# Optimization experiments

Hardware: AMD Instinct MI355X
Metric: run time of the kernel (lower is better)

The kernel has to match this reference:

```python
import jax, jax.numpy as jnp
import numpy as np

NT, NTR, NQ = 2048, 4096, 257  # time samples, traces, quantile knots


def cumtrapz(y, dx):
    # cumulative trapezoid along last axis, zero-prepended (preserve_dims=True)
    c = jnp.cumsum((y[..., 1:] + y[..., :-1]) * (0.5 * dx), axis=-1)
    return jnp.concatenate([jnp.zeros_like(y[..., :1]), c], axis=-1)


def trapz(y, dx):
    return (jnp.sum(y, axis=-1) - 0.5 * (y[..., 0] + y[..., -1])) * dx


def renorm(f, dx):
    # square + normalize to a pdf along time (standard W2-FWI renormalization)
    g = f * f
    return g / trapz(g, dx)[..., None]


def true_quantile(pdf, x, p, dx):
    # step-function quantile: invert clipped CDF via searchsorted per trace
    cdf = jnp.clip(cumtrapz(pdf, dx), 0.0, 1.0)  # [B, nt]
    idx = jax.vmap(lambda c: jnp.searchsorted(c, p))(cdf)  # [B, nq]
    idx = jnp.clip(idx, 0, x.shape[0] - 1)
    return x[idx]  # [B, nq]


def natural_cubic_coeffs(p, q):
    # batched natural cubic spline of q(p); knots p shared across batch
    h = p[1:] - p[:-1]                                 # [n-1]
    slope = (q[..., 1:] - q[..., :-1]) / h             # [B, n-1]
    rhs = 6.0 * (slope[..., 1:] - slope[..., :-1])     # [B, n-2]
    diag = 2.0 * (h[:-1] + h[1:])
    off = h[1:-1]
    T = jnp.diag(diag) + jnp.diag(off, 1) + jnp.diag(off, -1)  # [n-2, n-2], shared
    M_inner = jnp.linalg.solve(T, rhs[..., None])[..., 0]      # [B, n-2]
    z = jnp.zeros_like(q[..., :1])
    M = jnp.concatenate([z, M_inner, z], axis=-1)      # natural BCs: M0 = Mn = 0
    a = q[..., :-1]
    b = slope - h * (2.0 * M[..., :-1] + M[..., 1:]) / 6.0
    c = 0.5 * M[..., :-1]
    d = (M[..., 1:] - M[..., :-1]) / (6.0 * h)
    return a, b, c, d  # each [B, n-1]


def spline_eval(p, a, b, c, d, tq):
    # vectorized batched spline evaluation (replaces per-element Python loop)
    idx = jnp.clip(jnp.searchsorted(p, tq, side='left') - 1, 0, p.shape[0] - 2)
    frac = tq - p[idx]
    ga = jnp.take_along_axis(a, idx, axis=-1)
    gb = jnp.take_along_axis(b, idx, axis=-1)
    gc = jnp.take_along_axis(c, idx, axis=-1)
    gd = jnp.take_along_axis(d, idx, axis=-1)
    return ga + frac * (gb + frac * (gc + frac * gd))


def w2_forward(f, obs_data, t, p):
    dx = t[1] - t[0]
    # constructor-time part: quantile splines of observed data
    q = true_quantile(renorm(obs_data, dx), t, p, dx)   # [B, nq]
    a, b, c, d = natural_cubic_coeffs(p, q)
    # forward: CDF of synthetic, composed with observed quantile
    F = cumtrapz(renorm(f, dx), dx)                     # [B, nt]
    off_diag = spline_eval(p, a, b, c, d, F)            # [B, nt]
    diff = (t[None, :] - off_diag) ** 2
    integrated = trapz(diff * f, dx)                    # [B]
    return jnp.sum(integrated)


def setup_inputs() -> dict:
    key = jax.random.key(0)
    k1, k2 = jax.random.split(key)
    f = jax.random.normal(k1, (NTR, NT), dtype=jnp.float32)
    obs_data = jax.random.normal(k2, (NTR, NT), dtype=jnp.float32)
    t = jnp.linspace(0.0, 2.0, NT, dtype=jnp.float32)
    p = jnp.linspace(0.0, 1.0, NQ, dtype=jnp.float32)
    return {"f": f, "obs_data": obs_data, "t": t, "p": p}


def reference(f, obs_data, t, p):
    return w2_forward(f, obs_data, t, p)
```

## Files before the change

kernel.cpp:

```cpp
#include <hip/hip_runtime.h>

#define TPB 256
#define NT_ 2048
#define NQ_ 257
#define EPT 8
#define BW 16
#define BD (2*BW+1)
#define BAND_BYTES (BD*256*4)
#define H_P 0.00390625

__device__ __forceinline__ double shfl_down_f64(double x, int off) {
  union { double d; int i[2]; } u; u.d = x;
  u.i[0] = __shfl_down(u.i[0], off, 64);
  u.i[1] = __shfl_down(u.i[1], off, 64);
  return u.d;
}

__global__ void w2_setup(float* __restrict__ bandS) {
  __shared__ double sh_L[256];
  __shared__ double sh_winv[256];
  const int tid = threadIdx.x;
  if (tid < 255) {
    double d, dm;
    if (tid >= 20) {
      d = dm = 3.7320508075688772935;
    } else {
      d = 4.0; dm = 0.0;
      for (int i = 1; i <= tid; i++) { dm = d; d = 4.0 - 1.0 / d; }
    }
    sh_winv[tid] = 256.0 / d;
    sh_L[tid] = (tid == 0) ? 0.0 : 1.0 / dm;
  }
  __syncthreads();
  const int j = tid;
  const double H = H_P;
  if (j < 255) {
    double y[BW + 1];
    y[0] = 1.0;
    #pragma unroll
    for (int m = 1; m <= BW; m++) {
      int i = j + m;
      y[m] = (i <= 254) ? (-sh_L[i] * y[m - 1]) : 0.0;
    }
    double xn = 0.0;
    #pragma unroll
    for (int m = BW; m >= 0; m--) {
      int i = j + m;
      double val = 0.0;
      if (i <= 254) {
        double num = y[m] - ((i < 254) ? H * xn : 0.0);
        val = num * sh_winv[i];
        xn = val;
      }
      bandS[(m + BW) * 256 + j] = (float)val;
    }
    #pragma unroll
    for (int m = -1; m >= -BW; m--) {
      int i = j + m;
      double val = 0.0;
      if (i >= 0) {
        val = (-H * xn) * sh_winv[i];
        xn = val;
      }
      bandS[(m + BW) * 256 + j] = (float)val;
    }
  } else {
    for (int mm = 0; mm < BD; mm++) bandS[mm * 256 + j] = 0.0f;
  }
}

__global__ __launch_bounds__(TPB) void w2_main(
    const float* __restrict__ f, const float* __restrict__ obs,
    const float* __restrict__ t, const float* __restrict__ bandS,
    double* __restrict__ row_out) {
  __shared__ float s_q[NQ_];
  __shared__ float s_rhs[255 + 2 * BW];
  __shared__ float s_M[NQ_];
  __shared__ float4 s_coef[256];
  __shared__ float s_wf[4];
  __shared__ float s_wf2[4];
  __shared__ double s_wd[4];
  __shared__ double s_misc[2];

  const int tid = threadIdx.x;
  const int lane = tid & 63;
  const int wid = tid >> 6;
  const int row = blockIdx.x;
  const int base = tid * EPT;
  const int emax = (tid == TPB - 1) ? EPT - 1 : EPT;

  const double dx = (double)t[1] - (double)t[0];

  float tl[EPT + 1];
  {
    const float4 a = *reinterpret_cast<const float4*>(t + base);
    const float4 b = *reinterpret_cast<const float4*>(t + base + 4);
    tl[0] = a.x; tl[1] = a.y; tl[2] = a.z; tl[3] = a.w;
    tl[4] = b.x; tl[5] = b.y; tl[6] = b.z; tl[7] = b.w;
  }
  tl[EPT] = (tid < TPB - 1) ? t[base + EPT] : 0.0f;

  float sA[EPT];
  float ep = 0.0f;
  {
    const float* orow = obs + (size_t)row * NT_;
    float ov[EPT + 1];
    const float4 a = *reinterpret_cast<const float4*>(orow + base);
    const float4 b = *reinterpret_cast<const float4*>(orow + base + 4);
    ov[0] = a.x; ov[1] = a.y; ov[2] = a.z; ov[3] = a.w;
    ov[4] = b.x; ov[5] = b.y; ov[6] = b.z; ov[7] = b.w;
    ov[EPT] = (tid < TPB - 1) ? orow[base + EPT] : 0.0f;
    for (int k = 0; k < emax; k++) {
      sA[k] = ov[k] * ov[k] + ov[k + 1] * ov[k + 1];
      ep += sA[k];
    }
    if (emax < EPT) sA[EPT - 1] = 0.0f;
  }
  float v = ep;
  #pragma unroll
  for (int off = 1; off < 64; off <<= 1) {
    float w = __shfl_up(v, off, 64);
    if (lane >= off) v += w;
  }
  float excl = __shfl_up(v, 1, 64);
  if (lane == 0) excl = 0.0f;
  if (lane == 63) s_wf[wid] = v;
  __syncthreads();
  float woff = 0.0f, tot = 0.0f;
  #pragma unroll
  for (int w = 0; w < 4; w++) {
    float sw = s_wf[w];
    if (w < wid) woff += sw;
    tot += sw;
  }
  float run = woff + excl;
  float incl = woff + v;
  float inv = 1.0f / tot;

  {
    float cprev = fminf(run * inv, 1.0f);
    int j = (int)(cprev * 256.0f) + 1;
    float r = run;
    for (int k = 0; k < emax; k++) {
      float cu_uns = (k == emax - 1) ? incl : (r + sA[k]);
      r = cu_uns;
      float cuc = fminf(cu_uns * inv, 1.0f);
      int jh = (int)(cuc * 256.0f);
      float tq = tl[k + 1];
      for (; j <= jh; j++) s_q[j] = tq;
    }
    if (tid == 0) s_q[0] = tl[0];
    if (tid == TPB - 1) {
      float tq = tl[EPT - 1];
      for (; j <= 256; j++) s_q[j] = tq;
    }
  }

  const float* frow = f + (size_t)row * NT_;
  float fv[EPT + 1];
  {
    const float4 a = *reinterpret_cast<const float4*>(frow + base);
    const float4 b = *reinterpret_cast<const float4*>(frow + base + 4);
    fv[0] = a.x; fv[1] = a.y; fv[2] = a.z; fv[3] = a.w;
    fv[4] = b.x; fv[5] = b.y; fv[6] = b.z; fv[7] = b.w;
  }
  fv[EPT] = (tid < TPB - 1) ? frow[base + EPT] : 0.0f;

  float sB[EPT];
  float ep2 = 0.0f;
  for (int k = 0; k < emax; k++) {
    sB[k] = fv[k] * fv[k] + fv[k + 1] * fv[k + 1];
    ep2 += sB[k];
  }
  if (emax < EPT) sB[EPT - 1] = 0.0f;
  float v2 = ep2;
  #pragma unroll
  for (int off = 1; off < 64; off <<= 1) {
    float w = __shfl_up(v2, off, 64);
    if (lane >= off) v2 += w;
  }
  float excl2 = __shfl_up(v2, 1, 64);
  if (lane == 0) excl2 = 0.0f;
  if (lane == 63) s_wf2[wid] = v2;
  __syncthreads();

  float woff2 = 0.0f, tot2 = 0.0f;
  #pragma unroll
  for (int w = 0; w < 4; w++) {
    float sw = s_wf2[w];
    if (w < wid) woff2 += sw;
    tot2 += sw;
  }
  float run2 = woff2 + excl2;
  float inv2 = 1.0f / tot2;

  if (tid < 255) {
    float sl0 = (s_q[tid + 1] - s_q[tid]) * 256.0f;
    float sl1 = (s_q[tid + 2] - s_q[tid + 1]) * 256.0f;
    s_rhs[BW + tid] = 6.0f * (sl1 - sl0);
  }
  if (tid < BW) s_rhs[tid] = 0.0f;
  if (tid >= TPB - BW) s_rhs[tid + (2 * BW - 1)] = 0.0f;
  __syncthreads();

  float Mreg = 0.0f;
  if (tid < 255) {
    #pragma unroll 11
    for (int dd = 0; dd < BD; dd++)
      Mreg += bandS[dd * 256 + tid] * s_rhs[tid + dd];
  }
  if (tid < 255) s_M[tid + 1] = Mreg;
  if (tid == 0) { s_M[0] = 0.0f; s_M[256] = 0.0f; }
  __syncthreads();

  {
    const float h = (float)H_P;
    float q0 = s_q[tid], q1 = s_q[tid + 1];
    float Mi = s_M[tid], Mi1 = s_M[tid + 1];
    float sl = (q1 - q0) * 256.0f;
    float b = sl - h * (2.0f * Mi + Mi1) * (1.0f / 6.0f);
    float c = 0.5f * Mi;
    float d = (Mi1 - Mi) * (256.0f / 6.0f);
    s_coef[tid] = make_float4(q0, b, c, d);
  }
  __syncthreads();

  double wsum = 0.0;
  {
    float r2 = run2;
    #pragma unroll
    for (int k = 0; k < EPT; k++) {
      if (k > 0) r2 += sB[k - 1];
      float F = r2 * inv2;
      float G = F * 256.0f;
      int idx = (int)ceilf(G) - 1;
      if (idx < 0) idx = 0;
      if (idx > 255) idx = 255;
      float frac = F - (float)idx * (float)H_P;
      float4 cf = s_coef[idx];
      float val = cf.x + frac * (cf.y + frac * (cf.z + frac * cf.w));
      float diff = tl[k] - val;
      float wv = diff * diff * fv[k];
      if (tid == 0 && k == 0) s_misc[0] = (double)wv;
      if (tid == TPB - 1 && k == EPT - 1) s_misc[1] = (double)wv;
      wsum += (double)wv;
    }
  }
  double rv = wsum;
  #pragma unroll
  for (int off = 32; off >= 1; off >>= 1) rv += shfl_down_f64(rv, off);
  if (lane == 0) s_wd[wid] = rv;
  __syncthreads();
  if (tid == 0) {
    double totw = s_wd[0] + s_wd[1] + s_wd[2] + s_wd[3];
    row_out[row] = (totw - 0.5 * (s_misc[0] + s_misc[1])) * dx;
  }
}

__global__ void w2_reduce(const double* __restrict__ row_out, int ntr,
                          float* __restrict__ out) {
  __shared__ double s[TPB];
  int tid = threadIdx.x;
  double v = 0.0;
  for (int i = tid; i < ntr; i += TPB) v += row_out[i];
  s[tid] = v; __syncthreads();
  for (int off = TPB / 2; off > 0; off >>= 1) {
    if (tid < off) s[tid] += s[tid + off];
    __syncthreads();
  }
  if (tid == 0) out[0] = (float)s[0];
}

extern "C" void kernel_launch(void* const* d_in, const int* in_sizes, int n_in,
                              void* d_out, int out_size, void* d_ws, size_t ws_size,
                              hipStream_t stream) {
  const float* f   = (const float*)d_in[0];
  const float* obs = (const float*)d_in[1];
  const float* t   = (const float*)d_in[2];
  int nt = in_sizes[2];
  int ntr = in_sizes[0] / nt;

  float* bandS = (float*)d_ws;
  double* rows = (double*)((char*)d_ws + BAND_BYTES);

  hipLaunchKernelGGL(w2_setup, dim3(1), dim3(256), 0, stream, bandS);
  hipLaunchKernelGGL(w2_main, dim3(ntr), dim3(TPB), 0, stream,
                     f, obs, t, bandS, rows);
  hipLaunchKernelGGL(w2_reduce, dim3(1), dim3(TPB), 0, stream,
                     rows, ntr, (float*)d_out);
}
```

Measured before the change: 43.92 us.

## Process two traces per block and use shuffle-based final reduction

```diff
diff --git a/kernel.cpp b/kernel.cpp
--- a/kernel.cpp
+++ b/kernel.cpp
@@ -8,6 +8,7 @@
 #define BD (2*BW+1)
 #define BAND_BYTES (BD*256*4)
 #define H_P 0.00390625
+#define RTPB 1024
 
 __device__ __forceinline__ double shfl_down_f64(double x, int off) {
   union { double d; int i[2]; } u; u.d = x;
@@ -73,19 +74,19 @@
     const float* __restrict__ f, const float* __restrict__ obs,
     const float* __restrict__ t, const float* __restrict__ bandS,
     double* __restrict__ row_out) {
-  __shared__ float s_q[NQ_];
-  __shared__ float s_rhs[255 + 2 * BW];
-  __shared__ float s_M[NQ_];
-  __shared__ float4 s_coef[256];
-  __shared__ float s_wf[4];
-  __shared__ float s_wf2[4];
-  __shared__ double s_wd[4];
-  __shared__ double s_misc[2];
+  __shared__ float s_qA[NQ_], s_qB[NQ_];
+  __shared__ float s_rhsA[255 + 2 * BW], s_rhsB[255 + 2 * BW];
+  __shared__ float s_MA[NQ_], s_MB[NQ_];
+  __shared__ float4 s_coefA[256], s_coefB[256];
+  __shared__ float s_wfA[4], s_wfB[4], s_wf2A[4], s_wf2B[4];
+  __shared__ double s_wdA[4], s_wdB[4];
+  __shared__ double s_miscA[2], s_miscB[2];
 
   const int tid = threadIdx.x;
   const int lane = tid & 63;
   const int wid = tid >> 6;
-  const int row = blockIdx.x;
+  const int rowA = (int)blockIdx.x * 2;
+  const int rowB = rowA + 1;
   const int base = tid * EPT;
   const int emax = (tid == TPB - 1) ? EPT - 1 : EPT;
 
@@ -100,175 +101,242 @@
   }
   tl[EPT] = (tid < TPB - 1) ? t[base + EPT] : 0.0f;
 
-  float sA[EPT];
-  float ep = 0.0f;
-  {
-    const float* orow = obs + (size_t)row * NT_;
-    float ov[EPT + 1];
-    const float4 a = *reinterpret_cast<const float4*>(orow + base);
-    const float4 b = *reinterpret_cast<const float4*>(orow + base + 4);
-    ov[0] = a.x; ov[1] = a.y; ov[2] = a.z; ov[3] = a.w;
-    ov[4] = b.x; ov[5] = b.y; ov[6] = b.z; ov[7] = b.w;
-    ov[EPT] = (tid < TPB - 1) ? orow[base + EPT] : 0.0f;
+  float sAA[EPT], sAB[EPT];
+  float epA = 0.0f, epB = 0.0f;
+  {
+    const float* orA = obs + (size_t)rowA * NT_;
+    const float* orB = obs + (size_t)rowB * NT_;
+    float ovA[EPT + 1], ovB[EPT + 1];
+    {
+      const float4 a0 = *reinterpret_cast<const float4*>(orA + base);
+      const float4 a1 = *reinterpret_cast<const float4*>(orA + base + 4);
+      const float4 b0 = *reinterpret_cast<const float4*>(orB + base);
+      const float4 b1 = *reinterpret_cast<const float4*>(orB + base + 4);
+      ovA[0] = a0.x; ovA[1] = a0.y; ovA[2] = a0.z; ovA[3] = a0.w;
+      ovA[4] = a1.x; ovA[5] = a1.y; ovA[6] = a1.z; ovA[7] = a1.w;
+      ovB[0] = b0.x; ovB[1] = b0.y; ovB[2] = b0.z; ovB[3] = b0.w;
+      ovB[4] = b1.x; ovB[5] = b1.y; ovB[6] = b1.z; ovB[7] = b1.w;
+    }
+    ovA[EPT] = (tid < TPB - 1) ? orA[base + EPT] : 0.0f;
+    ovB[EPT] = (tid < TPB - 1) ? orB[base + EPT] : 0.0f;
     for (int k = 0; k < emax; k++) {
-      sA[k] = ov[k] * ov[k] + ov[k + 1] * ov[k + 1];
-      ep += sA[k];
-    }
-    if (emax < EPT) sA[EPT - 1] = 0.0f;
-  }
-  float v = ep;
+      sAA[k] = ovA[k] * ovA[k] + ovA[k + 1] * ovA[k + 1];
+      sAB[k] = ovB[k] * ovB[k] + ovB[k + 1] * ovB[k + 1];
+      epA += sAA[k];
+      epB += sAB[k];
+    }
+    if (emax < EPT) { sAA[EPT - 1] = 0.0f; sAB[EPT - 1] = 0.0f; }
+  }
+  float vA = epA, vB = epB;
   #pragma unroll
   for (int off = 1; off < 64; off <<= 1) {
-    float w = __shfl_up(v, off, 64);
-    if (lane >= off) v += w;
-  }
-  float excl = __shfl_up(v, 1, 64);
-  if (lane == 0) excl = 0.0f;
-  if (lane == 63) s_wf[wid] = v;
-  __syncthreads();
-  float woff = 0.0f, tot = 0.0f;
+    float wA = __shfl_up(vA, off, 64);
+    float wB = __shfl_up(vB, off, 64);
+    if (lane >= off) { vA += wA; vB += wB; }
+  }
+  float exclA = __shfl_up(vA, 1, 64);
+  float exclB = __shfl_up(vB, 1, 64);
+  if (lane == 0) { exclA = 0.0f; exclB = 0.0f; }
+  if (lane == 63) { s_wfA[wid] = vA; s_wfB[wid] = vB; }
+  __syncthreads();
+  float woffA = 0.0f, totA = 0.0f, woffB = 0.0f, totB = 0.0f;
   #pragma unroll
   for (int w = 0; w < 4; w++) {
-    float sw = s_wf[w];
-    if (w < wid) woff += sw;
-    tot += sw;
-  }
-  float run = woff + excl;
-  float incl = woff + v;
-  float inv = 1.0f / tot;
-
-  {
-    float cprev = fminf(run * inv, 1.0f);
+    float swA = s_wfA[w], swB = s_wfB[w];
+    if (w < wid) { woffA += swA; woffB += swB; }
+    totA += swA; totB += swB;
+  }
+  float runA = woffA + exclA, inclA = woffA + vA, invA = 1.0f / totA;
+  float runB = woffB + exclB, inclB = woffB + vB, invB = 1.0f / totB;
+
+  {
+    float cprev = fminf(runA * invA, 1.0f);
     int j = (int)(cprev * 256.0f) + 1;
-    float r = run;
+    float r = runA;
     for (int k = 0; k < emax; k++) {
-      float cu_uns = (k == emax - 1) ? incl : (r + sA[k]);
+      float cu_uns = (k == emax - 1) ? inclA : (r + sAA[k]);
       r = cu_uns;
-      float cuc = fminf(cu_uns * inv, 1.0f);
+      float cuc = fminf(cu_uns * invA, 1.0f);
       int jh = (int)(cuc * 256.0f);
       float tq = tl[k + 1];
-      for (; j <= jh; j++) s_q[j] = tq;
-    }
-    if (tid == 0) s_q[0] = tl[0];
+      for (; j <= jh; j++) s_qA[j] = tq;
+    }
+    if (tid == 0) s_qA[0] = tl[0];
     if (tid == TPB - 1) {
       float tq = tl[EPT - 1];
-      for (; j <= 256; j++) s_q[j] = tq;
-    }
-  }
-
-  const float* frow = f + (size_t)row * NT_;
-  float fv[EPT + 1];
-  {
-    const float4 a = *reinterpret_cast<const float4*>(frow + base);
-    const float4 b = *reinterpret_cast<const float4*>(frow + base + 4);
-    fv[0] = a.x; fv[1] = a.y; fv[2] = a.z; fv[3] = a.w;
-    fv[4] = b.x; fv[5] = b.y; fv[6] = b.z; fv[7] = b.w;
-  }
-  fv[EPT] = (tid < TPB - 1) ? frow[base + EPT] : 0.0f;
-
-  float sB[EPT];
-  float ep2 = 0.0f;
+      for (; j <= 256; j++) s_qA[j] = tq;
+    }
+  }
+  {
+    float cprev = fminf(runB * invB, 1.0f);
+    int j = (int)(cprev * 256.0f) + 1;
+    float r = runB;
+    for (int k = 0; k < emax; k++) {
+      float cu_uns = (k == emax - 1) ? inclB : (r + sAB[k]);
+      r = cu_uns;
+      float cuc = fminf(cu_uns * invB, 1.0f);
+      int jh = (int)(cuc * 256.0f);
+      float tq = tl[k + 1];
+      for (; j <= jh; j++) s_qB[j] = tq;
+    }
+    if (tid == 0) s_qB[0] = tl[0];
+    if (tid == TPB - 1) {
+      float tq = tl[EPT - 1];
+      for (; j <= 256; j++) s_qB[j] = tq;
+    }
+  }
+
+  const float* frA = f + (size_t)rowA * NT_;
+  const float* frB = f + (size_t)rowB * NT_;
+  float fvA[EPT + 1], fvB[EPT + 1];
+  {
+    const float4 a0 = *reinterpret_cast<const float4*>(frA + base);
+    const float4 a1 = *reinterpret_cast<const float4*>(frA + base + 4);
+    const float4 b0 = *reinterpret_cast<const float4*>(frB + base);
+    const float4 b1 = *reinterpret_cast<const float4*>(frB + base + 4);
+    fvA[0] = a0.x; fvA[1] = a0.y; fvA[2] = a0.z; fvA[3] = a0.w;
+    fvA[4] = a1.x; fvA[5] = a1.y; fvA[6] = a1.z; fvA[7] = a1.w;
+    fvB[0] = b0.x; fvB[1] = b0.y; fvB[2] = b0.z; fvB[3] = b0.w;
+    fvB[4] = b1.x; fvB[5] = b1.y; fvB[6] = b1.z; fvB[7] = b1.w;
+  }
+  fvA[EPT] = (tid < TPB - 1) ? frA[base + EPT] : 0.0f;
+  fvB[EPT] = (tid < TPB - 1) ? frB[base + EPT] : 0.0f;
+
+  float sBA[EPT], sBB[EPT];
+  float ep2A = 0.0f, ep2B = 0.0f;
   for (int k = 0; k < emax; k++) {
-    sB[k] = fv[k] * fv[k] + fv[k + 1] * fv[k + 1];
-    ep2 += sB[k];
-  }
-  if (emax < EPT) sB[EPT - 1] = 0.0f;
-  float v2 = ep2;
+    sBA[k] = fvA[k] * fvA[k] + fvA[k + 1] * fvA[k + 1];
+    sBB[k] = fvB[k] * fvB[k] + fvB[k + 1] * fvB[k + 1];
+    ep2A += sBA[k];
+    ep2B += sBB[k];
+  }
+  if (emax < EPT) { sBA[EPT - 1] = 0.0f; sBB[EPT - 1] = 0.0f; }
+  float v2A = ep2A, v2B = ep2B;
   #pragma unroll
   for (int off = 1; off < 64; off <<= 1) {
-    float w = __shfl_up(v2, off, 64);
-    if (lane >= off) v2 += w;
-  }
-  float excl2 = __shfl_up(v2, 1, 64);
-  if (lane == 0) excl2 = 0.0f;
-  if (lane == 63) s_wf2[wid] = v2;
-  __syncthreads();
-
-  float woff2 = 0.0f, tot2 = 0.0f;
+    float wA = __shfl_up(v2A, off, 64);
+    float wB = __shfl_up(v2B, off, 64);
+    if (lane >= off) { v2A += wA; v2B += wB; }
+  }
+  float excl2A = __shfl_up(v2A, 1, 64);
+  float excl2B = __shfl_up(v2B, 1, 64);
+  if (lane == 0) { excl2A = 0.0f; excl2B = 0.0f; }
+  if (lane == 63) { s_wf2A[wid] = v2A; s_wf2B[wid] = v2B; }
+  __syncthreads();
+
+  float woff2A = 0.0f, tot2A = 0.0f, woff2B = 0.0f, tot2B = 0.0f;
   #pragma unroll
   for (int w = 0; w < 4; w++) {
-    float sw = s_wf2[w];
-    if (w < wid) woff2 += sw;
-    tot2 += sw;
-  }
-  float run2 = woff2 + excl2;
-  float inv2 = 1.0f / tot2;
+    float swA = s_wf2A[w], swB = s_wf2B[w];
+    if (w < wid) { woff2A += swA; woff2B += swB; }
+    tot2A += swA; tot2B += swB;
+  }
+  float run2A = woff2A + excl2A, inv2A = 1.0f / tot2A;
+  float run2B = woff2B + excl2B, inv2B = 1.0f / tot2B;
 
   if (tid < 255) {
-    float sl0 = (s_q[tid + 1] - s_q[tid]) * 256.0f;
-    float sl1 = (s_q[tid + 2] - s_q[tid + 1]) * 256.0f;
-    s_rhs[BW + tid] = 6.0f * (sl1 - sl0);
-  }
-  if (tid < BW) s_rhs[tid] = 0.0f;
-  if (tid >= TPB - BW) s_rhs[tid + (2 * BW - 1)] = 0.0f;
-  __syncthreads();
-
-  float Mreg = 0.0f;
+    float sl0A = (s_qA[tid + 1] - s_qA[tid]) * 256.0f;
+    float sl1A = (s_qA[tid + 2] - s_qA[tid + 1]) * 256.0f;
+    s_rhsA[BW + tid] = 6.0f * (sl1A - sl0A);
+    float sl0B = (s_qB[tid + 1] - s_qB[tid]) * 256.0f;
+    float sl1B = (s_qB[tid + 2] - s_qB[tid + 1]) * 256.0f;
+    s_rhsB[BW + tid] = 6.0f * (sl1B - sl0B);
+  }
+  if (tid < BW) { s_rhsA[tid] = 0.0f; s_rhsB[tid] = 0.0f; }
+  if (tid >= TPB - BW) {
+    s_rhsA[tid + (2 * BW - 1)] = 0.0f;
+    s_rhsB[tid + (2 * BW - 1)] = 0.0f;
+  }
+  __syncthreads();
+
+  float MregA = 0.0f, MregB = 0.0f;
   if (tid < 255) {
     #pragma unroll 11
-    for (int dd = 0; dd < BD; dd++)
-      Mreg += bandS[dd * 256 + tid] * s_rhs[tid + dd];
-  }
-  if (tid < 255) s_M[tid + 1] = Mreg;
-  if (tid == 0) { s_M[0] = 0.0f; s_M[256] = 0.0f; }
+    for (int dd = 0; dd < BD; dd++) {
+      float w = bandS[dd * 256 + tid];
+      MregA += w * s_rhsA[tid + dd];
+      MregB += w * s_rhsB[tid + dd];
+    }
+  }
+  if (tid < 255) { s_MA[tid + 1] = MregA; s_MB[tid + 1] = MregB; }
+  if (tid == 0) { s_MA[0] = 0.0f; s_MA[256] = 0.0f; s_MB[0] = 0.0f; s_MB[256] = 0.0f; }
   __syncthreads();
 
   {
     const float h = (float)H_P;
-    float q0 = s_q[tid], q1 = s_q[tid + 1];
-    float Mi = s_M[tid], Mi1 = s_M[tid + 1];
-    float sl = (q1 - q0) * 256.0f;
-    float b = sl - h * (2.0f * Mi + Mi1) * (1.0f / 6.0f);
-    float c = 0.5f * Mi;
-    float d = (Mi1 - Mi) * (256.0f / 6.0f);
-    s_coef[tid] = make_float4(q0, b, c, d);
-  }
-  __syncthreads();
-
-  double wsum = 0.0;
-  {
-    float r2 = run2;
+    float q0A = s_qA[tid], q1A = s_qA[tid + 1];
+    float MiA = s_MA[tid], Mi1A = s_MA[tid + 1];
+    float slA = (q1A - q0A) * 256.0f;
+    float bA = slA - h * (2.0f * MiA + Mi1A) * (1.0f / 6.0f);
+    s_coefA[tid] = make_float4(q0A, bA, 0.5f * MiA, (Mi1A - MiA) * (256.0f / 6.0f));
+    float q0B = s_qB[tid], q1B = s_qB[tid + 1];
+    float MiB = s_MB[tid], Mi1B = s_MB[tid + 1];
+    float slB = (q1B - q0B) * 256.0f;
+    float bB = slB - h * (2.0f * MiB + Mi1B) * (1.0f / 6.0f);
+    s_coefB[tid] = make_float4(q0B, bB, 0.5f * MiB, (Mi1B - MiB) * (256.0f / 6.0f));
+  }
+  __syncthreads();
+
+  double wsumA = 0.0, wsumB = 0.0;
+  {
+    float r2A = run2A, r2B = run2B;
     #pragma unroll
     for (int k = 0; k < EPT; k++) {
-      if (k > 0) r2 += sB[k - 1];
-      float F = r2 * inv2;
-      float G = F * 256.0f;
-      int idx = (int)ceilf(G) - 1;
-      if (idx < 0) idx = 0;
-      if (idx > 255) idx = 255;
-      float frac = F - (float)idx * (float)H_P;
-      float4 cf = s_coef[idx];
-      float val = cf.x + frac * (cf.y + frac * (cf.z + frac * cf.w));
-      float diff = tl[k] - val;
-      float wv = diff * diff * fv[k];
-      if (tid == 0 && k == 0) s_misc[0] = (double)wv;
-      if (tid == TPB - 1 && k == EPT - 1) s_misc[1] = (double)wv;
-      wsum += (double)wv;
-    }
-  }
-  double rv = wsum;
-  #pragma unroll
-  for (int off = 32; off >= 1; off >>= 1) rv += shfl_down_f64(rv, off);
-  if (lane == 0) s_wd[wid] = rv;
+      if (k > 0) { r2A += sBA[k - 1]; r2B += sBB[k - 1]; }
+      float FA = r2A * inv2A;
+      float FB = r2B * inv2B;
+      int idxA = (int)ceilf(FA * 256.0f) - 1;
+      int idxB = (int)ceilf(FB * 256.0f) - 1;
+      if (idxA < 0) idxA = 0; if (idxA > 255) idxA = 255;
+      if (idxB < 0) idxB = 0; if (idxB > 255) idxB = 255;
+      float fracA = FA - (float)idxA * (float)H_P;
+      float fracB = FB - (float)idxB * (float)H_P;
+      float4 cfA = s_coefA[idxA];
+      float4 cfB = s_coefB[idxB];
+      float valA = cfA.x + fracA * (cfA.y + fracA * (cfA.z + fracA * cfA.w));
+      float valB = cfB.x + fracB * (cfB.y + fracB * (cfB.z + fracB * cfB.w));
+      float diffA = tl[k] - valA;
+      float diffB = tl[k] - valB;
+      float wvA = diffA * diffA * fvA[k];
+      float wvB = diffB * diffB * fvB[k];
+      if (tid == 0 && k == 0) { s_miscA[0] = (double)wvA; s_miscB[0] = (double)wvB; }
+      if (tid == TPB - 1 && k == EPT - 1) { s_miscA[1] = (double)wvA; s_miscB[1] = (double)wvB; }
+      wsumA += (double)wvA;
+      wsumB += (double)wvB;
+    }
+  }
+  double rA = wsumA, rB = wsumB;
+  #pragma unroll
+  for (int off = 32; off >= 1; off >>= 1) {
+    rA += shfl_down_f64(rA, off);
+    rB += shfl_down_f64(rB, off);
+  }
+  if (lane == 0) { s_wdA[wid] = rA; s_wdB[wid] = rB; }
   __syncthreads();
   if (tid == 0) {
-    double totw = s_wd[0] + s_wd[1] + s_wd[2] + s_wd[3];
-    row_out[row] = (totw - 0.5 * (s_misc[0] + s_misc[1])) * dx;
-  }
-}
-
-__global__ void w2_reduce(const double* __restrict__ row_out, int ntr,
-                          float* __restrict__ out) {
-  __shared__ double s[TPB];
-  int tid = threadIdx.x;
+    double totwA = s_wdA[0] + s_wdA[1] + s_wdA[2] + s_wdA[3];
+    double totwB = s_wdB[0] + s_wdB[1] + s_wdB[2] + s_wdB[3];
+    row_out[rowA] = (totwA - 0.5 * (s_miscA[0] + s_miscA[1])) * dx;
+    row_out[rowB] = (totwB - 0.5 * (s_miscB[0] + s_miscB[1])) * dx;
+  }
+}
+
+__global__ __launch_bounds__(RTPB) void w2_reduce(const double* __restrict__ row_out,
+                                                  int ntr, float* __restrict__ out) {
+  __shared__ double s[RTPB / 64];
+  int tid = threadIdx.x, lane = tid & 63, wid = tid >> 6;
   double v = 0.0;
-  for (int i = tid; i < ntr; i += TPB) v += row_out[i];
-  s[tid] = v; __syncthreads();
-  for (int off = TPB / 2; off > 0; off >>= 1) {
-    if (tid < off) s[tid] += s[tid + off];
-    __syncthreads();
-  }
-  if (tid == 0) out[0] = (float)s[0];
+  for (int i = tid; i < ntr; i += RTPB) v += row_out[i];
+  #pragma unroll
+  for (int off = 32; off >= 1; off >>= 1) v += shfl_down_f64(v, off);
+  if (lane == 0) s[wid] = v;
+  __syncthreads();
+  if (tid == 0) {
+    double tot = 0.0;
+    #pragma unroll
+    for (int i = 0; i < RTPB / 64; i++) tot += s[i];
+    out[0] = (float)tot;
+  }
 }
 
 extern "C" void kernel_launch(void* const* d_in, const int* in_sizes, int n_in,
@@ -284,8 +352,8 @@
   double* rows = (double*)((char*)d_ws + BAND_BYTES);
 
   hipLaunchKernelGGL(w2_setup, dim3(1), dim3(256), 0, stream, bandS);
-  hipLaunchKernelGGL(w2_main, dim3(ntr), dim3(TPB), 0, stream,
+  hipLaunchKernelGGL(w2_main, dim3(ntr / 2), dim3(TPB), 0, stream,
                      f, obs, t, bandS, rows);
-  hipLaunchKernelGGL(w2_reduce, dim3(1), dim3(TPB), 0, stream,
+  hipLaunchKernelGGL(w2_reduce, dim3(1), dim3(RTPB), 0, stream,
                      rows, ntr, (float*)d_out);
 }
```

After: 43.17 us. Within noise of the previous version (-1.7%).

## Map one trace per wavefront instead of one per block

Applied to the files above, without the earlier changes.

```diff
diff --git a/kernel.cpp b/kernel.cpp
--- a/kernel.cpp
+++ b/kernel.cpp
@@ -1,13 +1,15 @@
 #include <hip/hip_runtime.h>
 
-#define TPB 256
+#define WPB 4
+#define TPB (WPB * 64)
 #define NT_ 2048
-#define NQ_ 257
-#define EPT 8
+#define EPC 8
+#define NCH 4
 #define BW 16
 #define BD (2*BW+1)
 #define BAND_BYTES (BD*256*4)
-#define H_P 0.00390625
+#define H_P 0.00390625f
+#define RTPB 1024
 
 __device__ __forceinline__ double shfl_down_f64(double x, int off) {
   union { double d; int i[2]; } u; u.d = x;
@@ -33,7 +35,7 @@
   }
   __syncthreads();
   const int j = tid;
-  const double H = H_P;
+  const double H = (double)H_P;
   if (j < 255) {
     double y[BW + 1];
     y[0] = 1.0;
@@ -73,202 +75,224 @@
     const float* __restrict__ f, const float* __restrict__ obs,
     const float* __restrict__ t, const float* __restrict__ bandS,
     double* __restrict__ row_out) {
-  __shared__ float s_q[NQ_];
-  __shared__ float s_rhs[255 + 2 * BW];
-  __shared__ float s_M[NQ_];
-  __shared__ float4 s_coef[256];
-  __shared__ float s_wf[4];
-  __shared__ float s_wf2[4];
-  __shared__ double s_wd[4];
-  __shared__ double s_misc[2];
+  __shared__ float  s_q[WPB][260];
+  __shared__ float  s_rm[WPB][288];
+  __shared__ float4 s_coef[WPB][256];
 
   const int tid = threadIdx.x;
   const int lane = tid & 63;
   const int wid = tid >> 6;
-  const int row = blockIdx.x;
-  const int base = tid * EPT;
-  const int emax = (tid == TPB - 1) ? EPT - 1 : EPT;
-
+  const int row = (int)blockIdx.x * WPB + wid;
+
+  float*  q    = s_q[wid];
+  float*  rm   = s_rm[wid];
+  float4* coef = s_coef[wid];
+
+  const float* orow = obs + (size_t)row * NT_;
+  const float* frow = f + (size_t)row * NT_;
   const double dx = (double)t[1] - (double)t[0];
 
-  float tl[EPT + 1];
-  {
-    const float4 a = *reinterpret_cast<const float4*>(t + base);
-    const float4 b = *reinterpret_cast<const float4*>(t + base + 4);
-    tl[0] = a.x; tl[1] = a.y; tl[2] = a.z; tl[3] = a.w;
-    tl[4] = b.x; tl[5] = b.y; tl[6] = b.z; tl[7] = b.w;
-  }
-  tl[EPT] = (tid < TPB - 1) ? t[base + EPT] : 0.0f;
-
-  float sA[EPT];
-  float ep = 0.0f;
-  {
-    const float* orow = obs + (size_t)row * NT_;
-    float ov[EPT + 1];
-    const float4 a = *reinterpret_cast<const float4*>(orow + base);
-    const float4 b = *reinterpret_cast<const float4*>(orow + base + 4);
-    ov[0] = a.x; ov[1] = a.y; ov[2] = a.z; ov[3] = a.w;
-    ov[4] = b.x; ov[5] = b.y; ov[6] = b.z; ov[7] = b.w;
-    ov[EPT] = (tid < TPB - 1) ? orow[base + EPT] : 0.0f;
-    for (int k = 0; k < emax; k++) {
-      sA[k] = ov[k] * ov[k] + ov[k + 1] * ov[k + 1];
-      ep += sA[k];
-    }
-    if (emax < EPT) sA[EPT - 1] = 0.0f;
-  }
-  float v = ep;
+  float totA = 0.0f, totB = 0.0f;
+  for (int c = 0; c < NCH; c++) {
+    const int idx = c * 512 + lane * EPC;
+    const int km = (NT_ - 1 - idx < EPC) ? (NT_ - 1 - idx) : EPC;
+    float4 a0 = *reinterpret_cast<const float4*>(orow + idx);
+    float4 a1 = *reinterpret_cast<const float4*>(orow + idx + 4);
+    float4 b0 = *reinterpret_cast<const float4*>(frow + idx);
+    float4 b1 = *reinterpret_cast<const float4*>(frow + idx + 4);
+    float oe[9] = {a0.x,a0.y,a0.z,a0.w,a1.x,a1.y,a1.z,a1.w,
+                   (idx + 8 < NT_) ? orow[idx + 8] : 0.0f};
+    float fe[9] = {b0.x,b0.y,b0.z,b0.w,b1.x,b1.y,b1.z,b1.w,
+                   (idx + 8 < NT_) ? frow[idx + 8] : 0.0f};
+    #pragma unroll
+    for (int k = 0; k < EPC; k++) {
+      if (k < km) {
+        totA += oe[k]*oe[k] + oe[k+1]*oe[k+1];
+        totB += fe[k]*fe[k] + fe[k+1]*fe[k+1];
+      }
+    }
+  }
   #pragma unroll
   for (int off = 1; off < 64; off <<= 1) {
-    float w = __shfl_up(v, off, 64);
-    if (lane >= off) v += w;
-  }
-  float excl = __shfl_up(v, 1, 64);
-  if (lane == 0) excl = 0.0f;
-  if (lane == 63) s_wf[wid] = v;
-  __syncthreads();
-  float woff = 0.0f, tot = 0.0f;
-  #pragma unroll
-  for (int w = 0; w < 4; w++) {
-    float sw = s_wf[w];
-    if (w < wid) woff += sw;
-    tot += sw;
-  }
-  float run = woff + excl;
-  float incl = woff + v;
-  float inv = 1.0f / tot;
-
-  {
-    float cprev = fminf(run * inv, 1.0f);
+    totA += __shfl_xor(totA, off, 64);
+    totB += __shfl_xor(totB, off, 64);
+  }
+  const float invA = 1.0f / totA;
+  const float invB = 1.0f / totB;
+
+  float carry = 0.0f;
+  for (int c = 0; c < NCH; c++) {
+    const int idx = c * 512 + lane * EPC;
+    const int km = (NT_ - 1 - idx < EPC) ? (NT_ - 1 - idx) : EPC;
+    float4 a0 = *reinterpret_cast<const float4*>(orow + idx);
+    float4 a1 = *reinterpret_cast<const float4*>(orow + idx + 4);
+    float oe[9] = {a0.x,a0.y,a0.z,a0.w,a1.x,a1.y,a1.z,a1.w,
+                   (idx + 8 < NT_) ? orow[idx + 8] : 0.0f};
+    float4 t0 = *reinterpret_cast<const float4*>(t + idx);
+    float4 t1 = *reinterpret_cast<const float4*>(t + idx + 4);
+    float tq[9] = {t0.x,t0.y,t0.z,t0.w,t1.x,t1.y,t1.z,t1.w,
+                   (idx + 8 < NT_) ? t[idx + 8] : 0.0f};
+    float sA[EPC];
+    float ep = 0.0f;
+    #pragma unroll
+    for (int k = 0; k < EPC; k++) {
+      sA[k] = oe[k]*oe[k] + oe[k+1]*oe[k+1];
+      if (k < km) ep += sA[k];
+    }
+    float v = ep;
+    #pragma unroll
+    for (int off = 1; off < 64; off <<= 1) {
+      float w = __shfl_up(v, off, 64);
+      if (lane >= off) v += w;
+    }
+    float excl = __shfl_up(v, 1, 64);
+    if (lane == 0) excl = 0.0f;
+    const float run = carry + excl;
+    const float incl = carry + v;
+    float cprev = fminf(run * invA, 1.0f);
     int j = (int)(cprev * 256.0f) + 1;
     float r = run;
-    for (int k = 0; k < emax; k++) {
-      float cu_uns = (k == emax - 1) ? incl : (r + sA[k]);
-      r = cu_uns;
-      float cuc = fminf(cu_uns * inv, 1.0f);
-      int jh = (int)(cuc * 256.0f);
-      float tq = tl[k + 1];
-      for (; j <= jh; j++) s_q[j] = tq;
-    }
-    if (tid == 0) s_q[0] = tl[0];
-    if (tid == TPB - 1) {
-      float tq = tl[EPT - 1];
-      for (; j <= 256; j++) s_q[j] = tq;
-    }
-  }
-
-  const float* frow = f + (size_t)row * NT_;
-  float fv[EPT + 1];
-  {
-    const float4 a = *reinterpret_cast<const float4*>(frow + base);
-    const float4 b = *reinterpret_cast<const float4*>(frow + base + 4);
-    fv[0] = a.x; fv[1] = a.y; fv[2] = a.z; fv[3] = a.w;
-    fv[4] = b.x; fv[5] = b.y; fv[6] = b.z; fv[7] = b.w;
-  }
-  fv[EPT] = (tid < TPB - 1) ? frow[base + EPT] : 0.0f;
-
-  float sB[EPT];
-  float ep2 = 0.0f;
-  for (int k = 0; k < emax; k++) {
-    sB[k] = fv[k] * fv[k] + fv[k + 1] * fv[k + 1];
-    ep2 += sB[k];
-  }
-  if (emax < EPT) sB[EPT - 1] = 0.0f;
-  float v2 = ep2;
-  #pragma unroll
-  for (int off = 1; off < 64; off <<= 1) {
-    float w = __shfl_up(v2, off, 64);
-    if (lane >= off) v2 += w;
-  }
-  float excl2 = __shfl_up(v2, 1, 64);
-  if (lane == 0) excl2 = 0.0f;
-  if (lane == 63) s_wf2[wid] = v2;
-  __syncthreads();
-
-  float woff2 = 0.0f, tot2 = 0.0f;
-  #pragma unroll
-  for (int w = 0; w < 4; w++) {
-    float sw = s_wf2[w];
-    if (w < wid) woff2 += sw;
-    tot2 += sw;
-  }
-  float run2 = woff2 + excl2;
-  float inv2 = 1.0f / tot2;
-
-  if (tid < 255) {
-    float sl0 = (s_q[tid + 1] - s_q[tid]) * 256.0f;
-    float sl1 = (s_q[tid + 2] - s_q[tid + 1]) * 256.0f;
-    s_rhs[BW + tid] = 6.0f * (sl1 - sl0);
-  }
-  if (tid < BW) s_rhs[tid] = 0.0f;
-  if (tid >= TPB - BW) s_rhs[tid + (2 * BW - 1)] = 0.0f;
-  __syncthreads();
-
-  float Mreg = 0.0f;
-  if (tid < 255) {
-    #pragma unroll 11
-    for (int dd = 0; dd < BD; dd++)
-      Mreg += bandS[dd * 256 + tid] * s_rhs[tid + dd];
-  }
-  if (tid < 255) s_M[tid + 1] = Mreg;
-  if (tid == 0) { s_M[0] = 0.0f; s_M[256] = 0.0f; }
-  __syncthreads();
-
-  {
-    const float h = (float)H_P;
-    float q0 = s_q[tid], q1 = s_q[tid + 1];
-    float Mi = s_M[tid], Mi1 = s_M[tid + 1];
+    #pragma unroll
+    for (int k = 0; k < EPC; k++) {
+      if (k < km) {
+        float cu_uns = (k == km - 1) ? incl : (r + sA[k]);
+        r = cu_uns;
+        float cu = fminf(cu_uns * invA, 1.0f);
+        int jh = (int)(cu * 256.0f);
+        float tqv = tq[k + 1];
+        for (; j <= jh; j++) q[j] = tqv;
+      }
+    }
+    if (c == 0 && lane == 0) q[0] = tq[0];
+    if (c == NCH - 1 && lane == 63) {
+      float tqv = tq[7];
+      for (; j <= 256; j++) q[j] = tqv;
+    }
+    carry += __shfl(v, 63, 64);
+  }
+  __builtin_amdgcn_wave_barrier();
+
+  if (lane < BW) rm[lane] = 0.0f;
+  if (lane >= 48) rm[271 + (lane - 48)] = 0.0f;
+  #pragma unroll
+  for (int s = 0; s < 4; s++) {
+    int rr = lane + 64 * s;
+    if (rr < 255) {
+      float sl0 = (q[rr + 1] - q[rr]) * 256.0f;
+      float sl1 = (q[rr + 2] - q[rr + 1]) * 256.0f;
+      rm[BW + rr] = 6.0f * (sl1 - sl0);
+    }
+  }
+  __builtin_amdgcn_wave_barrier();
+
+  float Macc[4];
+  #pragma unroll
+  for (int s = 0; s < 4; s++) {
+    int rr = lane + 64 * s;
+    float acc = 0.0f;
+    if (rr < 255) {
+      #pragma unroll 11
+      for (int dd = 0; dd < BD; dd++)
+        acc += bandS[dd * 256 + rr] * rm[rr + dd];
+    }
+    Macc[s] = acc;
+  }
+  __builtin_amdgcn_wave_barrier();
+  #pragma unroll
+  for (int s = 0; s < 4; s++) {
+    int rr = lane + 64 * s;
+    if (rr < 255) rm[rr + 1] = Macc[s];
+  }
+  if (lane == 0) { rm[0] = 0.0f; rm[256] = 0.0f; }
+  __builtin_amdgcn_wave_barrier();
+
+  #pragma unroll
+  for (int s = 0; s < 4; s++) {
+    int i = lane + 64 * s;
+    float q0 = q[i], q1 = q[i + 1];
+    float Mi = rm[i], Mi1 = rm[i + 1];
     float sl = (q1 - q0) * 256.0f;
-    float b = sl - h * (2.0f * Mi + Mi1) * (1.0f / 6.0f);
-    float c = 0.5f * Mi;
-    float d = (Mi1 - Mi) * (256.0f / 6.0f);
-    s_coef[tid] = make_float4(q0, b, c, d);
-  }
-  __syncthreads();
-
+    float b = sl - H_P * (2.0f * Mi + Mi1) * (1.0f / 6.0f);
+    coef[i] = make_float4(q0, b, 0.5f * Mi, (Mi1 - Mi) * (256.0f / 6.0f));
+  }
+  __builtin_amdgcn_wave_barrier();
+
+  float carry2 = 0.0f;
   double wsum = 0.0;
-  {
-    float r2 = run2;
-    #pragma unroll
-    for (int k = 0; k < EPT; k++) {
+  float wv_first = 0.0f, wv_last = 0.0f;
+  for (int c = 0; c < NCH; c++) {
+    const int idx = c * 512 + lane * EPC;
+    const int km = (NT_ - 1 - idx < EPC) ? (NT_ - 1 - idx) : EPC;
+    float4 b0 = *reinterpret_cast<const float4*>(frow + idx);
+    float4 b1 = *reinterpret_cast<const float4*>(frow + idx + 4);
+    float fe[9] = {b0.x,b0.y,b0.z,b0.w,b1.x,b1.y,b1.z,b1.w,
+                   (idx + 8 < NT_) ? frow[idx + 8] : 0.0f};
+    float4 t0 = *reinterpret_cast<const float4*>(t + idx);
+    float4 t1 = *reinterpret_cast<const float4*>(t + idx + 4);
+    float tq[8] = {t0.x,t0.y,t0.z,t0.w,t1.x,t1.y,t1.z,t1.w};
+    float sB[EPC];
+    float ep2 = 0.0f;
+    #pragma unroll
+    for (int k = 0; k < EPC; k++) {
+      sB[k] = fe[k]*fe[k] + fe[k+1]*fe[k+1];
+      if (k < km) ep2 += sB[k];
+    }
+    float v = ep2;
+    #pragma unroll
+    for (int off = 1; off < 64; off <<= 1) {
+      float w = __shfl_up(v, off, 64);
+      if (lane >= off) v += w;
+    }
+    float excl = __shfl_up(v, 1, 64);
+    if (lane == 0) excl = 0.0f;
+    float r2 = carry2 + excl;
+    float csum = 0.0f;
+    #pragma unroll
+    for (int k = 0; k < EPC; k++) {
       if (k > 0) r2 += sB[k - 1];
-      float F = r2 * inv2;
+      float F = r2 * invB;
       float G = F * 256.0f;
-      int idx = (int)ceilf(G) - 1;
-      if (idx < 0) idx = 0;
-      if (idx > 255) idx = 255;
-      float frac = F - (float)idx * (float)H_P;
-      float4 cf = s_coef[idx];
+      int sg = (int)ceilf(G) - 1;
+      if (sg < 0) sg = 0;
+      if (sg > 255) sg = 255;
+      float frac = F - (float)sg * H_P;
+      float4 cf = coef[sg];
       float val = cf.x + frac * (cf.y + frac * (cf.z + frac * cf.w));
-      float diff = tl[k] - val;
-      float wv = diff * diff * fv[k];
-      if (tid == 0 && k == 0) s_misc[0] = (double)wv;
-      if (tid == TPB - 1 && k == EPT - 1) s_misc[1] = (double)wv;
-      wsum += (double)wv;
-    }
-  }
-  double rv = wsum;
-  #pragma unroll
-  for (int off = 32; off >= 1; off >>= 1) rv += shfl_down_f64(rv, off);
-  if (lane == 0) s_wd[wid] = rv;
+      float diff = tq[k] - val;
+      float wv = diff * diff * fe[k];
+      if (c == 0 && k == 0 && lane == 0) wv_first = wv;
+      if (c == NCH - 1 && k == EPC - 1 && lane == 63) wv_last = wv;
+      csum += wv;
+    }
+    wsum += (double)csum;
+    carry2 += __shfl(v, 63, 64);
+  }
+
+  double rtot = wsum;
+  #pragma unroll
+  for (int off = 32; off >= 1; off >>= 1) rtot += shfl_down_f64(rtot, off);
+  float wl = __shfl(wv_last, 63, 64);
+  if (lane == 0) {
+    row_out[row] = (rtot - 0.5 * ((double)wv_first + (double)wl)) * dx;
+  }
+}
+
+__global__ __launch_bounds__(RTPB) void w2_reduce(const double* __restrict__ row_out,
+                                                  int ntr, float* __restrict__ out) {
+  __shared__ double s[RTPB / 64];
+  int tid = threadIdx.x, lane = tid & 63, wid = tid >> 6;
+  double v = 0.0;
+  for (int i = tid; i < ntr; i += RTPB) v += row_out[i];
+  #pragma unroll
+  for (int off = 32; off >= 1; off >>= 1) v += shfl_down_f64(v, off);
+  if (lane == 0) s[wid] = v;
   __syncthreads();
   if (tid == 0) {
-    double totw = s_wd[0] + s_wd[1] + s_wd[2] + s_wd[3];
-    row_out[row] = (totw - 0.5 * (s_misc[0] + s_misc[1])) * dx;
-  }
-}
-
-__global__ void w2_reduce(const double* __restrict__ row_out, int ntr,
-                          float* __restrict__ out) {
-  __shared__ double s[TPB];
-  int tid = threadIdx.x;
-  double v = 0.0;
-  for (int i = tid; i < ntr; i += TPB) v += row_out[i];
-  s[tid] = v; __syncthreads();
-  for (int off = TPB / 2; off > 0; off >>= 1) {
-    if (tid < off) s[tid] += s[tid + off];
-    __syncthreads();
-  }
-  if (tid == 0) out[0] = (float)s[0];
+    double tot = 0.0;
+    #pragma unroll
+    for (int i = 0; i < RTPB / 64; i++) tot += s[i];
+    out[0] = (float)tot;
+  }
 }
 
 extern "C" void kernel_launch(void* const* d_in, const int* in_sizes, int n_in,
@@ -284,8 +308,8 @@
   double* rows = (double*)((char*)d_ws + BAND_BYTES);
 
   hipLaunchKernelGGL(w2_setup, dim3(1), dim3(256), 0, stream, bandS);
-  hipLaunchKernelGGL(w2_main, dim3(ntr), dim3(TPB), 0, stream,
+  hipLaunchKernelGGL(w2_main, dim3(ntr / WPB), dim3(TPB), 0, stream,
                      f, obs, t, bandS, rows);
-  hipLaunchKernelGGL(w2_reduce, dim3(1), dim3(TPB), 0, stream,
+  hipLaunchKernelGGL(w2_reduce, dim3(1), dim3(RTPB), 0, stream,
                      rows, ntr, (float*)d_out);
 }
```

New measurement: 48.63 us. +10.7%, slower.
